# Kernel tuning notes

Hardware: AMD Instinct MI355X
Metric: run time of the kernel (lower is better)

Reference implementation:

```python
import jax, jax.numpy as jnp
import numpy as np

B, N, D, H = 2, 2048, 1024, 16
HD = D // H
SCALE = HD ** -0.5


def setup_inputs() -> dict:
    key = jax.random.key(0)
    ks = jax.random.split(key, 9)
    s = D ** -0.5
    return {
        "x": jax.random.normal(ks[0], (B, N, D), dtype=jnp.float32),
        "Wq": jax.random.normal(ks[1], (D, D), dtype=jnp.float32) * s,
        "bq": jax.random.normal(ks[2], (D,), dtype=jnp.float32) * 0.01,
        "Wk": jax.random.normal(ks[3], (D, D), dtype=jnp.float32) * s,
        "bk": jax.random.normal(ks[4], (D,), dtype=jnp.float32) * 0.01,
        "Wv": jax.random.normal(ks[5], (D, D), dtype=jnp.float32) * s,
        "bv": jax.random.normal(ks[6], (D,), dtype=jnp.float32) * 0.01,
        "Wo": jax.random.normal(ks[7], (D, D), dtype=jnp.float32) * s,
        "bo": jax.random.normal(ks[8], (D,), dtype=jnp.float32) * 0.01,
    }


def reference(x, Wq, bq, Wk, bk, Wv, bv, Wo, bo):
    # Q/K/V projections (torch Linear: x @ W.T + b), split into heads: (B,H,N,HD)
    def proj(W, b):
        return (x @ W.T + b).reshape(B, N, H, HD).transpose(0, 2, 1, 3)

    q = proj(Wq, bq)
    k = proj(Wk, bk)
    v = proj(Wv, bv)
    # Scaled dot-product attention with explicit (B,H,N,N) scores
    scores = jnp.einsum("bhnd,bhmd->bhnm", q, k) * SCALE
    attn = jax.nn.softmax(scores, axis=-1)
    y = jnp.einsum("bhnm,bhmd->bhnd", attn, v)
    y = y.transpose(0, 2, 1, 3).reshape(B, N, D)
    # Output projection
    return y @ Wo.T + bo
```

## Files before the change

kernel.cpp:

```cpp
#include <hip/hip_runtime.h>

#define BB 2
#define NN 2048
#define DD 1024
#define HH 16
#define HD 64
#define SCALE 0.125f

typedef unsigned short u16;
typedef unsigned int u32;
typedef __attribute__((ext_vector_type(2))) unsigned int u32x2;
typedef __attribute__((ext_vector_type(4))) short short4v;
typedef __attribute__((ext_vector_type(8))) short short8;
typedef __attribute__((ext_vector_type(4))) float float4v;
typedef __attribute__((ext_vector_type(16))) float f32x16;

__device__ __forceinline__ float b2f(u16 u) {
    union { float f; u32 i; } x; x.i = ((u32)u) << 16; return x.f;
}
__device__ __forceinline__ u16 f2b(float f) {
    union { float f; u32 i; } x; x.f = f;
    u32 i = x.i;
    return (u16)((i + 0x7fffu + ((i >> 16) & 1u)) >> 16);
}

#if __has_builtin(__builtin_amdgcn_exp2f)
#define EXP2F(x) __builtin_amdgcn_exp2f(x)
#else
#define EXP2F(x) __expf((x) * 0.69314718055994531f)
#endif

#if __has_builtin(__builtin_amdgcn_rcpf)
#define RCPF(x) __builtin_amdgcn_rcpf(x)
#else
#define RCPF(x) (1.0f / (x))
#endif

#if __has_builtin(__builtin_amdgcn_permlane32_swap)
#define PSWAP(a, b, ra, rb)                                                  \
    { u32x2 _r = __builtin_amdgcn_permlane32_swap((a), (b), false, false);   \
      (ra) = _r[0]; (rb) = _r[1]; }
#else
#define PSWAP(a, b, ra, rb)                                                  \
    { u32 _xa = (u32)__shfl_xor((int)(a), 32, 64);                           \
      u32 _xb = (u32)__shfl_xor((int)(b), 32, 64);                           \
      (ra) = hi ? _xb : (a); (rb) = hi ? (b) : _xa; }
#endif

__device__ __forceinline__ u32 cvtpk(float a, float b) {
    u32 r;
    asm("v_cvt_pk_bf16_f32 %0, %1, %2" : "=v"(r) : "v"(a), "v"(b));
    return r;
}

__device__ __forceinline__ void gl_lds16(const u16* g, u16* l) {
    __builtin_amdgcn_global_load_lds(
        (__attribute__((address_space(1))) void*)(void*)g,
        (__attribute__((address_space(3))) void*)l, 16, 0, 0);
}

__global__ __launch_bounds__(256) void cvt_all(
    const float* __restrict__ x,
    const float* __restrict__ Wq, const float* __restrict__ Wk,
    const float* __restrict__ Wv, const float* __restrict__ Wo,
    u16* __restrict__ xb, u16* __restrict__ W4)
{
    int e = (blockIdx.x * 256 + threadIdx.x) * 8;
    const float* s;
    u16* d;
    if (e < 4194304) { s = x + e; d = xb + e; }
    else {
        int e2 = e - 4194304;
        int which = e2 >> 20;
        int off = e2 & 1048575;
        s = ((which == 0) ? Wq : (which == 1) ? Wk : (which == 2) ? Wv : Wo) + off;
        d = W4 + e2;
    }
    float4v a = *(const float4v*)s;
    float4v b = *(const float4v*)(s + 4);
    short8 r;
    r[0] = (short)f2b(a[0]); r[1] = (short)f2b(a[1]);
    r[2] = (short)f2b(a[2]); r[3] = (short)f2b(a[3]);
    r[4] = (short)f2b(b[0]); r[5] = (short)f2b(b[1]);
    r[6] = (short)f2b(b[2]); r[7] = (short)f2b(b[3]);
    *(short8*)d = r;
}

__global__ __launch_bounds__(256) void gemm_qkv(
    const u16* __restrict__ xb, const u16* __restrict__ W4,
    const float* __restrict__ bq, const float* __restrict__ bk,
    const float* __restrict__ bv,
    u16* __restrict__ Qo, u16* __restrict__ Ko, u16* __restrict__ Vt)
{
    const int id  = blockIdx.x;
    const int seq = (id & 7) * 64 + (id >> 3);
    const int tm = seq >> 4;
    const int tn = seq & 15;

    __shared__ u16 As[4][128 * 32];
    __shared__ u16 Bs[4][192 * 32];

    const int tid  = threadIdx.x;
    const int wave = tid >> 6, lane = tid & 63;
    const int wm = wave >> 1, wn = wave & 1;
    const int quad = lane >> 4, l16 = lane & 15;

    const int sr = tid >> 2, sc = tid & 3;
    const u16* gaA0 = &xb[(size_t)(tm * 128 + sr) * DD + sc * 8];
    const u16* gaA1 = gaA0 + (size_t)64 * DD;
    const u16* gbB0 = &W4[(size_t)(tn * 192 + sr) * DD + sc * 8];
    const u16* gbB1 = gbB0 + (size_t)64 * DD;
    const u16* gbB2 = gbB0 + (size_t)128 * DD;

    float4v acc[4][6] = {};

    #pragma unroll
    for (int s = 0; s < 3; ++s) {
        const int ks = s << 5;
        gl_lds16(gaA0 + ks, &As[s][tid * 8]);
        gl_lds16(gaA1 + ks, &As[s][(256 + tid) * 8]);
        gl_lds16(gbB0 + ks, &Bs[s][tid * 8]);
        gl_lds16(gbB1 + ks, &Bs[s][(256 + tid) * 8]);
        gl_lds16(gbB2 + ks, &Bs[s][(512 + tid) * 8]);
    }

    for (int it = 0; it < 32; ++it) {
        asm volatile("s_waitcnt vmcnt(10)" ::: "memory");
        __builtin_amdgcn_s_barrier();

        const int k3 = ((it + 3) & 31) << 5;
        const int b3 = (it + 3) & 3;
        gl_lds16(gaA0 + k3, &As[b3][tid * 8]);
        gl_lds16(gaA1 + k3, &As[b3][(256 + tid) * 8]);
        gl_lds16(gbB0 + k3, &Bs[b3][tid * 8]);
        gl_lds16(gbB1 + k3, &Bs[b3][(256 + tid) * 8]);
        gl_lds16(gbB2 + k3, &Bs[b3][(512 + tid) * 8]);

        const int cb = it & 3;
        short8 af[4], bf[6];
        #pragma unroll
        for (int mi = 0; mi < 4; ++mi)
            af[mi] = *(const short8*)&As[cb][(wm * 64 + mi * 16 + l16) * 32 + quad * 8];
        #pragma unroll
        for (int ni = 0; ni < 6; ++ni)
            bf[ni] = *(const short8*)&Bs[cb][(wn * 96 + ni * 16 + l16) * 32 + quad * 8];

        #pragma unroll
        for (int mi = 0; mi < 4; ++mi)
            #pragma unroll
            for (int ni = 0; ni < 6; ++ni)
                acc[mi][ni] = __builtin_amdgcn_mfma_f32_16x16x32_bf16(
                    af[mi], bf[ni], acc[mi][ni], 0, 0, 0);
    }
    asm volatile("s_waitcnt vmcnt(0)" ::: "memory");

    #pragma unroll
    for (int mi = 0; mi < 4; ++mi) {
        #pragma unroll
        for (int ni = 0; ni < 6; ++ni) {
            int cc = tn * 192 + wn * 96 + ni * 16 + l16;
            int matf = cc >> 10;
            int cin = cc & 1023;
            int h = cin >> 6, hd = cin & 63;
            float bb = ((matf == 0) ? bq : (matf == 1) ? bk : bv)[cin];
            if (matf == 2) {
                short4v v4;
                #pragma unroll
                for (int rr = 0; rr < 4; ++rr)
                    v4[rr] = (short)f2b(acc[mi][ni][rr] + bb);
                int R0 = tm * 128 + wm * 64 + mi * 16 + quad * 4;
                int b = R0 >> 11, n = R0 & 2047;
                *(short4v*)&Vt[(((size_t)(b * HH + h)) * HD + hd) * NN + n] = v4;
            } else {
                u16* Out = (matf == 0) ? Qo : Ko;
                #pragma unroll
                for (int rr = 0; rr < 4; ++rr) {
                    int R = tm * 128 + wm * 64 + mi * 16 + quad * 4 + rr;
                    int b = R >> 11, n = R & 2047;
                    Out[(((size_t)(b * HH + h)) * NN + n) * HD + hd] =
                        f2b(acc[mi][ni][rr] + bb);
                }
            }
        }
    }
}

__global__ __launch_bounds__(512) void gemm_out(
    const u16* __restrict__ A, const u16* __restrict__ W,
    const float* __restrict__ bias, float* __restrict__ Out)
{
    const int tn = blockIdx.x;
    const int tm = blockIdx.y;

    __shared__ u16 As[4][128 * 32];
    __shared__ u16 Bs[4][128 * 32];

    const int tid  = threadIdx.x;
    const int wave = tid >> 6, lane = tid & 63;
    const int wm = wave >> 2, wn = wave & 3;
    const int quad = lane >> 4, l16 = lane & 15;

    const int sr = tid >> 2, sc = tid & 3;
    const u16* ga = &A[(size_t)(tm * 128 + sr) * DD + sc * 8];
    const u16* gb = &W[(size_t)(tn * 128 + sr) * DD + sc * 8];

    float4v acc[4][2] = {};

    #pragma unroll
    for (int s = 0; s < 3; ++s) {
        const int ks = s << 5;
        gl_lds16(ga + ks, &As[s][tid * 8]);
        gl_lds16(gb + ks, &Bs[s][tid * 8]);
    }

    for (int it = 0; it < 32; ++it) {
        asm volatile("s_waitcnt vmcnt(4)" ::: "memory");
        __builtin_amdgcn_s_barrier();

        const int k3 = ((it + 3) & 31) << 5;
        const int b3 = (it + 3) & 3;
        gl_lds16(ga + k3, &As[b3][tid * 8]);
        gl_lds16(gb + k3, &Bs[b3][tid * 8]);

        const int cb = it & 3;
        short8 af[4], bf[2];
        #pragma unroll
        for (int mi = 0; mi < 4; ++mi)
            af[mi] = *(const short8*)&As[cb][(wm * 64 + mi * 16 + l16) * 32 + quad * 8];
        #pragma unroll
        for (int ni = 0; ni < 2; ++ni)
            bf[ni] = *(const short8*)&Bs[cb][(wn * 32 + ni * 16 + l16) * 32 + quad * 8];

        #pragma unroll
        for (int mi = 0; mi < 4; ++mi)
            #pragma unroll
            for (int ni = 0; ni < 2; ++ni)
                acc[mi][ni] = __builtin_amdgcn_mfma_f32_16x16x32_bf16(
                    af[mi], bf[ni], acc[mi][ni], 0, 0, 0);
    }
    asm volatile("s_waitcnt vmcnt(0)" ::: "memory");

    #pragma unroll
    for (int mi = 0; mi < 4; ++mi) {
        #pragma unroll
        for (int ni = 0; ni < 2; ++ni) {
            int cc = tn * 128 + wn * 32 + ni * 16 + l16;
            float bv_ = bias[cc];
            #pragma unroll
            for (int rr = 0; rr < 4; ++rr) {
                int R = tm * 128 + wm * 64 + mi * 16 + quad * 4 + rr;
                Out[(size_t)R * DD + cc] = acc[mi][ni][rr] + bv_;
            }
        }
    }
}

__global__ __launch_bounds__(256) void attn_mfma(
    const u16* __restrict__ Q, const u16* __restrict__ K,
    const u16* __restrict__ Vt, u16* __restrict__ Y)
{
    const int id   = blockIdx.x;
    const int xcd  = id & 7;
    const int slot = id >> 3;
    const int bh   = (xcd << 2) | (slot & 3);
    const int qb   = slot >> 2;

    const int tid  = threadIdx.x;
    const int wave = tid >> 6, lane = tid & 63;
    const int l31  = lane & 31, hi = lane >> 5;

    const u16* __restrict__ Qb = Q + (size_t)bh * NN * HD;
    const u16* __restrict__ Kb = K + (size_t)bh * NN * HD;
    const u16* __restrict__ Vb = Vt + (size_t)bh * HD * NN;

    __shared__ u16 Ks[4][64 * 64];
    __shared__ u16 Vs[4][64 * 64];

    short8 qf[4];
    {
        int qrow = qb * 128 + wave * 32 + l31;
        #pragma unroll
        for (int c = 0; c < 4; ++c) {
            short8 t = *(const short8*)&Qb[(size_t)qrow * HD + c * 16 + hi * 8];
            #pragma unroll
            for (int j = 0; j < 8; ++j)
                qf[c][j] = (short)f2b(b2f((u16)t[j]) * SCALE);
        }
    }

    short8 onesB;
    #pragma unroll
    for (int j = 0; j < 8; ++j) onesB[j] = (short)0x3F80;

    f32x16 oc[2] = {};
    f32x16 la = {};

    const int srow = tid >> 3, sslot = tid & 7;
    const int oA = (sslot + srow) & 7;
    const int oB = (sslot + srow + 32) & 7;

    #pragma unroll
    for (int s = 0; s < 3; ++s) {
        const int ks = s * 64;
        gl_lds16(&Kb[(size_t)(ks + srow) * HD + oA * 8],      &Ks[s][tid * 8]);
        gl_lds16(&Kb[(size_t)(ks + srow + 32) * HD + oB * 8], &Ks[s][(256 + tid) * 8]);
        gl_lds16(&Vb[(size_t)srow * NN + ks + oA * 8],        &Vs[s][tid * 8]);
        gl_lds16(&Vb[(size_t)(srow + 32) * NN + ks + oB * 8], &Vs[s][(256 + tid) * 8]);
    }

    for (int it = 0; it < 32; ++it) {
        asm volatile("s_waitcnt vmcnt(8)" ::: "memory");
        __builtin_amdgcn_s_barrier();

        const int k3 = ((it + 3) & 31) * 64;
        const int b3 = (it + 3) & 3;
        gl_lds16(&Kb[(size_t)(k3 + srow) * HD + oA * 8],      &Ks[b3][tid * 8]);
        gl_lds16(&Kb[(size_t)(k3 + srow + 32) * HD + oB * 8], &Ks[b3][(256 + tid) * 8]);
        gl_lds16(&Vb[(size_t)srow * NN + k3 + oA * 8],        &Vs[b3][tid * 8]);
        gl_lds16(&Vb[(size_t)(srow + 32) * NN + k3 + oB * 8], &Vs[b3][(256 + tid) * 8]);

        const int cur = it & 3;

        f32x16 st[2];
        __builtin_amdgcn_s_setprio(1);
        #pragma unroll
        for (int kt = 0; kt < 2; ++kt) {
            f32x16 z = {};
            const int row = kt * 32 + l31;
            #pragma unroll
            for (int c = 0; c < 4; ++c) {
                short8 kf = *(const short8*)
                    &Ks[cur][row * 64 + ((2 * c + hi - row) & 7) * 8];
                z = __builtin_amdgcn_mfma_f32_32x32x16_bf16(kf, qf[c], z, 0, 0, 0);
            }
            st[kt] = z;
        }
        __builtin_amdgcn_s_setprio(0);

        u32 pk0[8], pk1[8];
        #pragma unroll
        for (int i = 0; i < 8; ++i) {
            float a0 = EXP2F(__builtin_fmaf(st[0][2 * i],     1.44269504f, -11.5415603f));
            float a1 = EXP2F(__builtin_fmaf(st[0][2 * i + 1], 1.44269504f, -11.5415603f));
            pk0[i] = cvtpk(a0, a1);
            float b0 = EXP2F(__builtin_fmaf(st[1][2 * i],     1.44269504f, -11.5415603f));
            float b1 = EXP2F(__builtin_fmaf(st[1][2 * i + 1], 1.44269504f, -11.5415603f));
            pk1[i] = cvtpk(b0, b1);
        }

        short8 pa[4];
        {
            union { u32 w[4]; short8 s; } lo, hi_;
            PSWAP(pk0[0], pk0[2], lo.w[0], lo.w[2]);
            PSWAP(pk0[1], pk0[3], lo.w[1], lo.w[3]);
            PSWAP(pk0[4], pk0[6], hi_.w[0], hi_.w[2]);
            PSWAP(pk0[5], pk0[7], hi_.w[1], hi_.w[3]);
            pa[0] = lo.s; pa[1] = hi_.s;
            PSWAP(pk1[0], pk1[2], lo.w[0], lo.w[2]);
            PSWAP(pk1[1], pk1[3], lo.w[1], lo.w[3]);
            PSWAP(pk1[4], pk1[6], hi_.w[0], hi_.w[2]);
            PSWAP(pk1[5], pk1[7], hi_.w[1], hi_.w[3]);
            pa[2] = lo.s; pa[3] = hi_.s;
        }

        __builtin_amdgcn_s_setprio(1);
        #pragma unroll
        for (int ks = 0; ks < 4; ++ks)
            la = __builtin_amdgcn_mfma_f32_32x32x16_bf16(pa[ks], onesB, la, 0, 0, 0);
        #pragma unroll
        for (int ks = 0; ks < 4; ++ks) {
            #pragma unroll
            for (int ht = 0; ht < 2; ++ht) {
                const int row = ht * 32 + l31;
                short8 vf = *(const short8*)
                    &Vs[cur][row * 64 + ((2 * ks + hi - row) & 7) * 8];
                oc[ht] = __builtin_amdgcn_mfma_f32_32x32x16_bf16(pa[ks], vf, oc[ht], 0, 0, 0);
            }
        }
        __builtin_amdgcn_s_setprio(0);
    }
    asm volatile("s_waitcnt vmcnt(0)" ::: "memory");

    const int b = bh >> 4, h = bh & 15;
    #pragma unroll
    for (int r = 0; r < 16; ++r) {
        const int n = qb * 128 + wave * 32 + (r & 3) + 8 * (r >> 2) + 4 * hi;
        const float iv = RCPF(la[r]);
        #pragma unroll
        for (int ht = 0; ht < 2; ++ht) {
            const int col = h * HD + ht * 32 + l31;
            Y[((size_t)(b * NN + n)) * DD + col] = f2b(oc[ht][r] * iv);
        }
    }
}

extern "C" void kernel_launch(void* const* d_in, const int* in_sizes, int n_in,
                              void* d_out, int out_size, void* d_ws, size_t ws_size,
                              hipStream_t stream) {
    const float* x  = (const float*)d_in[0];
    const float* Wq = (const float*)d_in[1];
    const float* bq = (const float*)d_in[2];
    const float* Wk = (const float*)d_in[3];
    const float* bk = (const float*)d_in[4];
    const float* Wv = (const float*)d_in[5];
    const float* bv = (const float*)d_in[6];
    const float* Wo = (const float*)d_in[7];
    const float* bo = (const float*)d_in[8];
    float* out = (float*)d_out;

    const size_t M1 = 1024 * 1024;
    u16* base = (u16*)d_ws;
    u16* xb  = base;
    u16* W4  = base + 4 * M1;
    u16* Wob = W4 + 3 * M1;
    u16* Qw  = base + 8 * M1;
    u16* Kw  = base + 12 * M1;
    u16* Vtw = base + 16 * M1;
    u16* Yw  = xb;

    cvt_all<<<dim3(4096), 256, 0, stream>>>(x, Wq, Wk, Wv, Wo, xb, W4);

    gemm_qkv<<<dim3(512), 256, 0, stream>>>(xb, W4, bq, bk, bv, Qw, Kw, Vtw);

    attn_mfma<<<dim3(512), 256, 0, stream>>>(Qw, Kw, Vtw, Yw);

    gemm_out<<<dim3(8, 32), 512, 0, stream>>>(Yw, Wob, bo, out);
}
```

Before: 217.5 us.

## Restructure QKV GEMM with 256x192 tiles, swizzled LDS, interleaved load/MFMA schedule

The QKV projection GEMM now uses 512-thread blocks computing 256x192 tiles with a K-step of 64. It double-buffers LDS with an XOR-swizzled layout, and global-to-LDS loads are interleaved between MFMA phases under s_setprio. The output GEMM also gets an XOR swizzle on its LDS layout and priority raising around its MFMAs. These changes target LDS bank conflicts and the poor overlap of memory and compute in the projection GEMMs. In exchange there is higher register and LDS pressure and only 256 blocks, which may underfill the GPU.

```diff
diff --git a/kernel.cpp b/kernel.cpp
--- a/kernel.cpp
+++ b/kernel.cpp
@@ -27,7 +27,7 @@
 #if __has_builtin(__builtin_amdgcn_exp2f)
 #define EXP2F(x) __builtin_amdgcn_exp2f(x)
 #else
-#define EXP2F(x) __expf((x) * 0.69314718055994531f)
+#define EXP2F(x) exp2f(x)
 #endif
 
 #if __has_builtin(__builtin_amdgcn_rcpf)
@@ -86,103 +86,168 @@
     *(short8*)d = r;
 }
 
-__global__ __launch_bounds__(256) void gemm_qkv(
+__global__ __launch_bounds__(512) void gemm_qkv(
     const u16* __restrict__ xb, const u16* __restrict__ W4,
     const float* __restrict__ bq, const float* __restrict__ bk,
     const float* __restrict__ bv,
     u16* __restrict__ Qo, u16* __restrict__ Ko, u16* __restrict__ Vt)
 {
     const int id  = blockIdx.x;
-    const int seq = (id & 7) * 64 + (id >> 3);
+    const int seq = (id & 7) * 32 + (id >> 3);
     const int tm = seq >> 4;
     const int tn = seq & 15;
 
-    __shared__ u16 As[4][128 * 32];
-    __shared__ u16 Bs[4][192 * 32];
-
-    const int tid  = threadIdx.x;
+    __shared__ u16 As[2][256 * 64];
+    __shared__ u16 Bs[2][192 * 64];
+
+    const int tid = threadIdx.x;
     const int wave = tid >> 6, lane = tid & 63;
-    const int wm = wave >> 1, wn = wave & 1;
+    const int wm = wave >> 2, wn = wave & 3;
     const int quad = lane >> 4, l16 = lane & 15;
-
-    const int sr = tid >> 2, sc = tid & 3;
-    const u16* gaA0 = &xb[(size_t)(tm * 128 + sr) * DD + sc * 8];
-    const u16* gaA1 = gaA0 + (size_t)64 * DD;
-    const u16* gbB0 = &W4[(size_t)(tn * 192 + sr) * DD + sc * 8];
-    const u16* gbB1 = gbB0 + (size_t)64 * DD;
-    const u16* gbB2 = gbB0 + (size_t)128 * DD;
-
-    float4v acc[4][6] = {};
-
-    #pragma unroll
-    for (int s = 0; s < 3; ++s) {
-        const int ks = s << 5;
-        gl_lds16(gaA0 + ks, &As[s][tid * 8]);
-        gl_lds16(gaA1 + ks, &As[s][(256 + tid) * 8]);
-        gl_lds16(gbB0 + ks, &Bs[s][tid * 8]);
-        gl_lds16(gbB1 + ks, &Bs[s][(256 + tid) * 8]);
-        gl_lds16(gbB2 + ks, &Bs[s][(512 + tid) * 8]);
-    }
-
-    for (int it = 0; it < 32; ++it) {
-        asm volatile("s_waitcnt vmcnt(10)" ::: "memory");
-        __builtin_amdgcn_s_barrier();
-
-        const int k3 = ((it + 3) & 31) << 5;
-        const int b3 = (it + 3) & 3;
-        gl_lds16(gaA0 + k3, &As[b3][tid * 8]);
-        gl_lds16(gaA1 + k3, &As[b3][(256 + tid) * 8]);
-        gl_lds16(gbB0 + k3, &Bs[b3][tid * 8]);
-        gl_lds16(gbB1 + k3, &Bs[b3][(256 + tid) * 8]);
-        gl_lds16(gbB2 + k3, &Bs[b3][(512 + tid) * 8]);
-
-        const int cb = it & 3;
-        short8 af[4], bf[6];
-        #pragma unroll
-        for (int mi = 0; mi < 4; ++mi)
-            af[mi] = *(const short8*)&As[cb][(wm * 64 + mi * 16 + l16) * 32 + quad * 8];
-        #pragma unroll
-        for (int ni = 0; ni < 6; ++ni)
-            bf[ni] = *(const short8*)&Bs[cb][(wn * 96 + ni * 16 + l16) * 32 + quad * 8];
-
-        #pragma unroll
-        for (int mi = 0; mi < 4; ++mi)
-            #pragma unroll
-            for (int ni = 0; ni < 6; ++ni)
-                acc[mi][ni] = __builtin_amdgcn_mfma_f32_16x16x32_bf16(
-                    af[mi], bf[ni], acc[mi][ni], 0, 0, 0);
+    const int l7 = l16 & 7;
+
+    const int sr8  = tid >> 3;
+    const int slot = (tid & 7) ^ (sr8 & 7);
+    const u16* gA = &xb[(size_t)(tm * 256 + sr8) * DD + slot * 8];
+    const u16* gB = &W4[(size_t)(tn * 192 + sr8) * DD + slot * 8];
+
+#define STAGE_A(bf_, g_, kt_) \
+    gl_lds16(gA + (size_t)(g_) * 64 * DD + (kt_), &As[bf_][(tid + (g_) * 512) * 8])
+#define STAGE_B(bf_, g_, kt_) \
+    gl_lds16(gB + (size_t)(g_) * 64 * DD + (kt_), &Bs[bf_][(tid + (g_) * 512) * 8])
+
+    const int sA0 = ((0 + quad) ^ l7) * 8;
+    const int sA1 = ((4 + quad) ^ l7) * 8;
+
+    float4v acc[8][3] = {};
+    short8 aF[4][2], bF[3][2];
+
+    #pragma unroll
+    for (int g = 0; g < 4; ++g) STAGE_A(0, g, 0);
+    #pragma unroll
+    for (int g = 0; g < 3; ++g) STAGE_B(0, g, 0);
+    #pragma unroll
+    for (int g = 0; g < 4; ++g) STAGE_A(1, g, 64);
+    #pragma unroll
+    for (int g = 0; g < 3; ++g) STAGE_B(1, g, 64);
+
+    for (int it = 0; it < 8; ++it) {
+        #pragma unroll
+        for (int h = 0; h < 2; ++h) {
+            const int cb  = h;
+            const int ktn = ((2 * it + 2 + h) & 15) * 64;
+
+            asm volatile("s_waitcnt vmcnt(7)" ::: "memory");
+            __builtin_amdgcn_s_barrier();
+            #pragma unroll
+            for (int mi = 0; mi < 4; ++mi) {
+                const int ro = (wm * 128 + mi * 16 + l16) * 64;
+                aF[mi][0] = *(const short8*)&As[cb][ro + sA0];
+                aF[mi][1] = *(const short8*)&As[cb][ro + sA1];
+            }
+            #pragma unroll
+            for (int ni = 0; ni < 3; ++ni) {
+                const int ro = (wn * 48 + ni * 16 + l16) * 64;
+                bF[ni][0] = *(const short8*)&Bs[cb][ro + sA0];
+                bF[ni][1] = *(const short8*)&Bs[cb][ro + sA1];
+            }
+            asm volatile("s_waitcnt lgkmcnt(0)" ::: "memory");
+            __builtin_amdgcn_s_setprio(1);
+            #pragma unroll
+            for (int mi = 0; mi < 4; ++mi)
+                #pragma unroll
+                for (int ni = 0; ni < 2; ++ni) {
+                    acc[mi][ni] = __builtin_amdgcn_mfma_f32_16x16x32_bf16(
+                        aF[mi][0], bF[ni][0], acc[mi][ni], 0, 0, 0);
+                    acc[mi][ni] = __builtin_amdgcn_mfma_f32_16x16x32_bf16(
+                        aF[mi][1], bF[ni][1], acc[mi][ni], 0, 0, 0);
+                }
+            __builtin_amdgcn_s_setprio(0);
+            __builtin_amdgcn_s_barrier();
+
+            STAGE_A(cb, 0, ktn);
+            STAGE_A(cb, 2, ktn);
+            __builtin_amdgcn_s_setprio(1);
+            #pragma unroll
+            for (int mi = 0; mi < 4; ++mi) {
+                acc[mi][2] = __builtin_amdgcn_mfma_f32_16x16x32_bf16(
+                    aF[mi][0], bF[2][0], acc[mi][2], 0, 0, 0);
+                acc[mi][2] = __builtin_amdgcn_mfma_f32_16x16x32_bf16(
+                    aF[mi][1], bF[2][1], acc[mi][2], 0, 0, 0);
+            }
+            __builtin_amdgcn_s_setprio(0);
+            __builtin_amdgcn_s_barrier();
+
+            #pragma unroll
+            for (int mi = 0; mi < 4; ++mi) {
+                const int ro = (wm * 128 + (mi + 4) * 16 + l16) * 64;
+                aF[mi][0] = *(const short8*)&As[cb][ro + sA0];
+                aF[mi][1] = *(const short8*)&As[cb][ro + sA1];
+            }
+            STAGE_B(cb, 0, ktn);
+            STAGE_B(cb, 1, ktn);
+            STAGE_B(cb, 2, ktn);
+            asm volatile("s_waitcnt lgkmcnt(0)" ::: "memory");
+            __builtin_amdgcn_s_setprio(1);
+            #pragma unroll
+            for (int mi = 0; mi < 4; ++mi)
+                #pragma unroll
+                for (int ni = 0; ni < 2; ++ni) {
+                    acc[mi + 4][ni] = __builtin_amdgcn_mfma_f32_16x16x32_bf16(
+                        aF[mi][0], bF[ni][0], acc[mi + 4][ni], 0, 0, 0);
+                    acc[mi + 4][ni] = __builtin_amdgcn_mfma_f32_16x16x32_bf16(
+                        aF[mi][1], bF[ni][1], acc[mi + 4][ni], 0, 0, 0);
+                }
+            __builtin_amdgcn_s_setprio(0);
+            __builtin_amdgcn_s_barrier();
+
+            STAGE_A(cb, 1, ktn);
+            STAGE_A(cb, 3, ktn);
+            __builtin_amdgcn_s_setprio(1);
+            #pragma unroll
+            for (int mi = 0; mi < 4; ++mi) {
+                acc[mi + 4][2] = __builtin_amdgcn_mfma_f32_16x16x32_bf16(
+                    aF[mi][0], bF[2][0], acc[mi + 4][2], 0, 0, 0);
+                acc[mi + 4][2] = __builtin_amdgcn_mfma_f32_16x16x32_bf16(
+                    aF[mi][1], bF[2][1], acc[mi + 4][2], 0, 0, 0);
+            }
+            __builtin_amdgcn_s_setprio(0);
+            __builtin_amdgcn_s_barrier();
+        }
     }
     asm volatile("s_waitcnt vmcnt(0)" ::: "memory");
 
     #pragma unroll
-    for (int mi = 0; mi < 4; ++mi) {
-        #pragma unroll
-        for (int ni = 0; ni < 6; ++ni) {
-            int cc = tn * 192 + wn * 96 + ni * 16 + l16;
+    for (int mi = 0; mi < 8; ++mi) {
+        #pragma unroll
+        for (int ni = 0; ni < 3; ++ni) {
+            int cc = tn * 192 + wn * 48 + ni * 16 + l16;
             int matf = cc >> 10;
             int cin = cc & 1023;
-            int h = cin >> 6, hd = cin & 63;
+            int h2 = cin >> 6, hd = cin & 63;
             float bb = ((matf == 0) ? bq : (matf == 1) ? bk : bv)[cin];
             if (matf == 2) {
                 short4v v4;
                 #pragma unroll
                 for (int rr = 0; rr < 4; ++rr)
                     v4[rr] = (short)f2b(acc[mi][ni][rr] + bb);
-                int R0 = tm * 128 + wm * 64 + mi * 16 + quad * 4;
+                int R0 = tm * 256 + wm * 128 + mi * 16 + quad * 4;
                 int b = R0 >> 11, n = R0 & 2047;
-                *(short4v*)&Vt[(((size_t)(b * HH + h)) * HD + hd) * NN + n] = v4;
+                *(short4v*)&Vt[(((size_t)(b * HH + h2)) * HD + hd) * NN + n] = v4;
             } else {
                 u16* Out = (matf == 0) ? Qo : Ko;
                 #pragma unroll
                 for (int rr = 0; rr < 4; ++rr) {
-                    int R = tm * 128 + wm * 64 + mi * 16 + quad * 4 + rr;
+                    int R = tm * 256 + wm * 128 + mi * 16 + quad * 4 + rr;
                     int b = R >> 11, n = R & 2047;
-                    Out[(((size_t)(b * HH + h)) * NN + n) * HD + hd] =
+                    Out[(((size_t)(b * HH + h2)) * NN + n) * HD + hd] =
                         f2b(acc[mi][ni][rr] + bb);
                 }
             }
         }
     }
+#undef STAGE_A
+#undef STAGE_B
 }
 
 __global__ __launch_bounds__(512) void gemm_out(
@@ -201,8 +266,11 @@
     const int quad = lane >> 4, l16 = lane & 15;
 
     const int sr = tid >> 2, sc = tid & 3;
-    const u16* ga = &A[(size_t)(tm * 128 + sr) * DD + sc * 8];
-    const u16* gb = &W[(size_t)(tn * 128 + sr) * DD + sc * 8];
+    const int scs = sc ^ ((sr >> 1) & 3);
+    const u16* ga = &A[(size_t)(tm * 128 + sr) * DD + scs * 8];
+    const u16* gb = &W[(size_t)(tn * 128 + sr) * DD + scs * 8];
+
+    const int qsw8 = (quad ^ ((l16 >> 1) & 3)) * 8;
 
     float4v acc[4][2] = {};
 
@@ -226,17 +294,19 @@
         short8 af[4], bf[2];
         #pragma unroll
         for (int mi = 0; mi < 4; ++mi)
-            af[mi] = *(const short8*)&As[cb][(wm * 64 + mi * 16 + l16) * 32 + quad * 8];
+            af[mi] = *(const short8*)&As[cb][(wm * 64 + mi * 16 + l16) * 32 + qsw8];
         #pragma unroll
         for (int ni = 0; ni < 2; ++ni)
-            bf[ni] = *(const short8*)&Bs[cb][(wn * 32 + ni * 16 + l16) * 32 + quad * 8];
-
+            bf[ni] = *(const short8*)&Bs[cb][(wn * 32 + ni * 16 + l16) * 32 + qsw8];
+
+        __builtin_amdgcn_s_setprio(1);
         #pragma unroll
         for (int mi = 0; mi < 4; ++mi)
             #pragma unroll
             for (int ni = 0; ni < 2; ++ni)
                 acc[mi][ni] = __builtin_amdgcn_mfma_f32_16x16x32_bf16(
                     af[mi], bf[ni], acc[mi][ni], 0, 0, 0);
+        __builtin_amdgcn_s_setprio(0);
     }
     asm volatile("s_waitcnt vmcnt(0)" ::: "memory");
 
@@ -420,7 +490,7 @@
 
     cvt_all<<<dim3(4096), 256, 0, stream>>>(x, Wq, Wk, Wv, Wo, xb, W4);
 
-    gemm_qkv<<<dim3(512), 256, 0, stream>>>(xb, W4, bq, bk, bv, Qw, Kw, Vtw);
+    gemm_qkv<<<dim3(256), 512, 0, stream>>>(xb, W4, bq, bk, bv, Qw, Kw, Vtw);
 
     attn_mfma<<<dim3(512), 256, 0, stream>>>(Qw, Kw, Vtw, Yw);
 
```

Measured after the change: 188.0 us. -13.6%, faster.
